# Kernel optimization log

Hardware: AMD Instinct MI355X
Metric: run time of the kernel (lower is better)

Reference implementation:

```python
import jax, jax.numpy as jnp
import numpy as np

B, T, S, E, H = 2, 1024, 1024, 1024, 16
D = E // H  # head_dim = 64
SCALING = D ** -0.5


def setup_inputs() -> dict:
    key = jax.random.key(0)
    ks = jax.random.split(key, 14)
    inv = 1.0 / np.sqrt(E)
    inp = {
        "query": jax.random.normal(ks[0], (B, T, E), jnp.float32),
        "key": jax.random.normal(ks[1], (B, S, E), jnp.float32),
        "value": jax.random.normal(ks[2], (B, S, E), jnp.float32),
        "key_padding_mask": jax.random.bernoulli(ks[3], 0.1, (B, S)),
        "attn_bias": jax.random.normal(ks[4], (B * H, T, S), jnp.float32),
        "Wq": jax.random.uniform(ks[5], (E, E), jnp.float32, -inv, inv),
        "bq": jax.random.uniform(ks[6], (E,), jnp.float32, -inv, inv),
        "Wk": jax.random.uniform(ks[7], (E, E), jnp.float32, -inv, inv),
        "bk": jax.random.uniform(ks[8], (E,), jnp.float32, -inv, inv),
        "Wv": jax.random.uniform(ks[9], (E, E), jnp.float32, -inv, inv),
        "bv": jax.random.uniform(ks[10], (E,), jnp.float32, -inv, inv),
        "Wo": jax.random.uniform(ks[11], (E, E), jnp.float32, -inv, inv),
        "bo": jax.random.uniform(ks[12], (E,), jnp.float32, -inv, inv),
    }
    return inp


def reference(query, key, value, key_padding_mask, attn_bias,
              Wq, bq, Wk, bk, Wv, bv, Wo, bo):
    # Projections (torch Linear: x @ W.T + b)
    q = query @ Wq.T + bq  # [B, T, E]
    k = key @ Wk.T + bk    # [B, S, E]
    v = value @ Wv.T + bv  # [B, S, E]
    # Split heads -> [B, H, L, D]
    q = q.reshape(B, T, H, D).transpose(0, 2, 1, 3) * SCALING
    k = k.reshape(B, S, H, D).transpose(0, 2, 1, 3)
    v = v.reshape(B, S, H, D).transpose(0, 2, 1, 3)
    # Scores [B, H, T, S]
    attn_weights = jnp.einsum('bhtd,bhsd->bhts', q, k)
    # key_padding_mask: True means masked -> -inf (applied BEFORE bias add)
    attn_weights = jnp.where(key_padding_mask[:, None, None, :], -jnp.inf, attn_weights)
    # softmax_dropout with additive bias (eval mode: dropout is identity)
    attn_weights = attn_weights + attn_bias.reshape(B, H, T, S)
    attn = jax.nn.softmax(attn_weights, axis=-1)
    o = jnp.einsum('bhts,bhsd->bhtd', attn, v)  # [B, H, T, D]
    o = o.transpose(0, 2, 1, 3).reshape(B, T, E)
    return o @ Wo.T + bo
```

## Files before the change

### kernel.cpp

```cpp
#include <hip/hip_runtime.h>
#include <math.h>
#include <stdint.h>

#define B_ 2
#define T_ 1024
#define S_ 1024
#define E_ 1024
#define H_ 16
#define SCALING_ 0.125f

typedef short bf16x8 __attribute__((ext_vector_type(8)));
typedef float f32x4 __attribute__((ext_vector_type(4)));
typedef unsigned short us8 __attribute__((ext_vector_type(8)));

__device__ __forceinline__ unsigned short f2bf(float x) {
    unsigned int u = __float_as_uint(x);
    return (unsigned short)((u + 0x7fffu + ((u >> 16) & 1u)) >> 16);
}
__device__ __forceinline__ float bf2f(unsigned short h) {
    return __uint_as_float(((unsigned int)h) << 16);
}
__device__ __forceinline__ void split_bf(float x, unsigned short& hh, unsigned short& ll) {
    hh = f2bf(x);
    ll = f2bf(x - bf2f(hh));
}
__device__ __forceinline__ void gl_lds16(const void* g, void* l) {
    __builtin_amdgcn_global_load_lds(
        (const __attribute__((address_space(1))) unsigned int*)g,
        (__attribute__((address_space(3))) unsigned int*)l, 16, 0, 0);
}
template <int CTRL>
__device__ __forceinline__ float dpp_ror(float x) {
    int v = __builtin_amdgcn_update_dpp(0, __float_as_int(x), CTRL, 0xf, 0xf, true);
    return __int_as_float(v);
}

__global__ void mask_detect_kernel(const unsigned int* __restrict__ p,
                                   int* __restrict__ mode_out) {
    __shared__ int gt1_s, oddnz_s;
    if (threadIdx.x == 0) { gt1_s = 0; oddnz_s = 0; }
    __syncthreads();
    int gt1 = 0;
    for (int i = threadIdx.x; i < 512; i += 256)
        if (p[i] > 1u) gt1 = 1;
    if (gt1) atomicOr(&gt1_s, 1);
    __syncthreads();
    if (gt1_s == 0) {
        int oddnz = 0;
        for (int i = threadIdx.x; i < 2048; i += 256)
            if ((i & 1) && p[i] != 0u) oddnz = 1;
        if (oddnz) atomicOr(&oddnz_s, 1);
    }
    __syncthreads();
    if (threadIdx.x == 0)
        *mode_out = gt1_s ? 1 : (oddnz_s ? 0 : 2);
}

__global__ void mask_norm_kernel(const void* __restrict__ p,
                                 const int* __restrict__ mode_p,
                                 int* __restrict__ mout) {
    int i = blockIdx.x * 256 + threadIdx.x;
    int mode = *mode_p;
    int v;
    if (mode == 1)      v = (int)((const unsigned char*)p)[i];
    else if (mode == 2) v = ((const int*)p)[2 * i];
    else                v = ((const int*)p)[i];
    mout[i] = v;
}

__global__ __launch_bounds__(256) void conv_split7_kernel(
    const float* __restrict__ Wq, const float* __restrict__ Wk,
    const float* __restrict__ Wv, const float* __restrict__ Wo,
    const float* __restrict__ xq, const float* __restrict__ xk,
    const float* __restrict__ xv,
    unsigned short* __restrict__ Wqh, unsigned short* __restrict__ Wql,
    unsigned short* __restrict__ Wkh, unsigned short* __restrict__ Wkl,
    unsigned short* __restrict__ Wvh, unsigned short* __restrict__ Wvl,
    unsigned short* __restrict__ Woh, unsigned short* __restrict__ Wol,
    unsigned short* __restrict__ xqh, unsigned short* __restrict__ xql,
    unsigned short* __restrict__ xkh, unsigned short* __restrict__ xkl,
    unsigned short* __restrict__ xvh, unsigned short* __restrict__ xvl) {
    int bid = blockIdx.x;
    const float* src; unsigned short* dh; unsigned short* dl; int lb;
    if (bid < 2048) {
        int w = bid >> 9; lb = bid & 511;
        if (w == 0)      { src = Wq; dh = Wqh; dl = Wql; }
        else if (w == 1) { src = Wk; dh = Wkh; dl = Wkl; }
        else if (w == 2) { src = Wv; dh = Wvh; dl = Wvl; }
        else             { src = Wo; dh = Woh; dl = Wol; }
    } else {
        int a = (bid - 2048) >> 10; lb = (bid - 2048) & 1023;
        if (a == 0)      { src = xq; dh = xqh; dl = xql; }
        else if (a == 1) { src = xk; dh = xkh; dl = xkl; }
        else             { src = xv; dh = xvh; dl = xvl; }
    }
    int i = (lb * 256 + threadIdx.x) * 8;
    float4 a4 = *(const float4*)&src[i];
    float4 b4 = *(const float4*)&src[i + 4];
    float v[8] = {a4.x, a4.y, a4.z, a4.w, b4.x, b4.y, b4.z, b4.w};
    us8 vh, vl;
#pragma unroll
    for (int j = 0; j < 8; j++) {
        unsigned short hh, ll;
        split_bf(v[j], hh, ll);
        vh[j] = hh; vl[j] = ll;
    }
    *(us8*)&dh[i] = vh;
    *(us8*)&dl[i] = vl;
}

template <int BM, int NW, int N, int K, int ROWBIAS, int SPLITOUT>
__device__ __forceinline__ void gemm_body2(
    int bid,
    const unsigned short* __restrict__ Ahg, const unsigned short* __restrict__ Alg,
    const unsigned short* __restrict__ Bhg, const unsigned short* __restrict__ Blg,
    const float* __restrict__ bias,
    unsigned short* __restrict__ outh, unsigned short* __restrict__ outl,
    float* __restrict__ outf, float alpha, unsigned short* lds) {
    const int tid = threadIdx.x;
    const int lane = tid & 63;
    const int wave = tid >> 6;
    const int wm = wave >> 1, wn = wave & 1;
    const int bn = bid % (N / 64);
    const int bm = bid / (N / 64);
    const int m0 = bm * BM, n0 = bn * 64;
    constexpr int NT = K / 32;
    constexpr int ABUF = BM * 32;
    constexpr int BUFE = 2 * ABUF + 4096;
    const int arow = tid >> 2, aoct = tid & 3;

    f32x4 acc[2][2];
#pragma unroll
    for (int i = 0; i < 2; i++)
#pragma unroll
        for (int j = 0; j < 2; j++) acc[i][j] = (f32x4){0.f, 0.f, 0.f, 0.f};

    auto stage = [&](int k0, unsigned short* buf) {
        int ao2 = aoct ^ ((arow >> 1) & 3);
        size_t ga = (size_t)(m0 + arow) * K + k0 + ao2 * 8;
        gl_lds16(&Ahg[ga], &buf[arow * 32 + aoct * 8]);
        gl_lds16(&Alg[ga], &buf[ABUF + arow * 32 + aoct * 8]);
        if (NW == 8) {
            int bslot = tid & 255;
            int brow = bslot >> 2, boct = bslot & 3;
            int bo2 = boct ^ ((brow >> 1) & 3);
            size_t gb = (size_t)(n0 + brow) * K + k0 + bo2 * 8;
            const unsigned short* src = (tid < 256) ? Bhg : Blg;
            gl_lds16(&src[gb],
                     &buf[2 * ABUF + (tid < 256 ? 0 : 2048) + bslot * 8]);
        } else {
            int brow = tid >> 2, boct = tid & 3;
            int bo2 = boct ^ ((brow >> 1) & 3);
            size_t gb = (size_t)(n0 + brow) * K + k0 + bo2 * 8;
            gl_lds16(&Bhg[gb], &buf[2 * ABUF + tid * 8]);
            gl_lds16(&Blg[gb], &buf[2 * ABUF + 2048 + tid * 8]);
        }
    };

    stage(0, lds);
    asm volatile("s_waitcnt vmcnt(0)" ::: "memory");
    __syncthreads();

    for (int t = 0; t < NT; t++) {
        unsigned short* cur = lds + (t & 1) * BUFE;
        unsigned short* nxt = lds + ((t & 1) ^ 1) * BUFE;
        if (t + 1 < NT) stage((t + 1) * 32, nxt);

        bf16x8 af[2][2], bf_[2][2];
#pragma unroll
        for (int nj = 0; nj < 2; nj++) {
            int rowB = wn * 32 + nj * 16 + (lane & 15);
            int ch = (lane >> 4) ^ ((rowB >> 1) & 3);
            bf_[nj][0] = *(const bf16x8*)&cur[2 * ABUF + rowB * 32 + ch * 8];
            bf_[nj][1] = *(const bf16x8*)&cur[2 * ABUF + 2048 + rowB * 32 + ch * 8];
        }
#pragma unroll
        for (int mi = 0; mi < 2; mi++) {
            int rowA = wm * 32 + mi * 16 + (lane & 15);
            int ch = (lane >> 4) ^ ((rowA >> 1) & 3);
            af[mi][0] = *(const bf16x8*)&cur[rowA * 32 + ch * 8];
            af[mi][1] = *(const bf16x8*)&cur[ABUF + rowA * 32 + ch * 8];
        }
#pragma unroll
        for (int mi = 0; mi < 2; mi++)
#pragma unroll
            for (int nj = 0; nj < 2; nj++) {
                acc[mi][nj] = __builtin_amdgcn_mfma_f32_16x16x32_bf16(af[mi][0], bf_[nj][0], acc[mi][nj], 0, 0, 0);
                acc[mi][nj] = __builtin_amdgcn_mfma_f32_16x16x32_bf16(af[mi][1], bf_[nj][0], acc[mi][nj], 0, 0, 0);
                acc[mi][nj] = __builtin_amdgcn_mfma_f32_16x16x32_bf16(af[mi][0], bf_[nj][1], acc[mi][nj], 0, 0, 0);
            }

        asm volatile("s_waitcnt vmcnt(0)" ::: "memory");
        __syncthreads();
    }

    float bcol[2];
    if (!ROWBIAS) {
#pragma unroll
        for (int nj = 0; nj < 2; nj++)
            bcol[nj] = bias[n0 + wn * 32 + nj * 16 + (lane & 15)];
    }
#pragma unroll
    for (int mi = 0; mi < 2; mi++) {
#pragma unroll
        for (int r = 0; r < 4; r++) {
            int row = m0 + wm * 32 + mi * 16 + (lane >> 4) * 4 + r;
            float brow = ROWBIAS ? bias[row] : 0.f;
#pragma unroll
            for (int nj = 0; nj < 2; nj++) {
                int col = n0 + wn * 32 + nj * 16 + (lane & 15);
                float v = alpha * (acc[mi][nj][r] + (ROWBIAS ? brow : bcol[nj]));
                if (SPLITOUT) {
                    unsigned short hh, ll;
                    split_bf(v, hh, ll);
                    outh[(size_t)row * N + col] = hh;
                    outl[(size_t)row * N + col] = ll;
                } else {
                    outf[(size_t)row * N + col] = v;
                }
            }
        }
    }
}

__global__ __launch_bounds__(512, 4) void proj_fused_kernel(
    const unsigned short* __restrict__ xqh, const unsigned short* __restrict__ xql,
    const unsigned short* __restrict__ xkh, const unsigned short* __restrict__ xkl,
    const unsigned short* __restrict__ xvh, const unsigned short* __restrict__ xvl,
    const unsigned short* __restrict__ Wqh, const unsigned short* __restrict__ Wql,
    const unsigned short* __restrict__ Wkh, const unsigned short* __restrict__ Wkl,
    const unsigned short* __restrict__ Wvh, const unsigned short* __restrict__ Wvl,
    const float* __restrict__ bq, const float* __restrict__ bk,
    const float* __restrict__ bv_,
    unsigned short* __restrict__ qh, unsigned short* __restrict__ ql,
    unsigned short* __restrict__ kh, unsigned short* __restrict__ kl,
    unsigned short* __restrict__ vth, unsigned short* __restrict__ vtl) {
    __shared__ __align__(16) unsigned short lds[2 * (2 * 128 * 32 + 4096)];
    int op = blockIdx.x >> 8;
    int bid = blockIdx.x & 255;
    if (op == 0)
        gemm_body2<128, 8, 1024, 1024, 0, 1>(bid, xqh, xql, Wqh, Wql, bq,
                                             qh, ql, nullptr, SCALING_, lds);
    else if (op == 1)
        gemm_body2<128, 8, 1024, 1024, 0, 1>(bid, xkh, xkl, Wkh, Wkl, bk,
                                             kh, kl, nullptr, 1.f, lds);
    else
        gemm_body2<128, 8, 2048, 1024, 1, 1>(bid, Wvh, Wvl, xvh, xvl, bv_,
                                             vth, vtl, nullptr, 1.f, lds);
}

__global__ __launch_bounds__(256) void gemm_out_kernel(
    const unsigned short* __restrict__ oh, const unsigned short* __restrict__ ol,
    const unsigned short* __restrict__ Woh, const unsigned short* __restrict__ Wol,
    const float* __restrict__ bo, float* __restrict__ out) {
    __shared__ __align__(16) unsigned short lds[2 * (2 * 64 * 32 + 4096)];
    gemm_body2<64, 4, 1024, 1024, 0, 0>(blockIdx.x, oh, ol, Woh, Wol, bo,
                                        nullptr, nullptr, out, 1.f, lds);
}

__global__ __launch_bounds__(256) void flash_kernel(
    const unsigned short* __restrict__ qh, const unsigned short* __restrict__ ql,
    const unsigned short* __restrict__ kh, const unsigned short* __restrict__ kl,
    const unsigned short* __restrict__ vth, const unsigned short* __restrict__ vtl,
    const float* __restrict__ bias, const int* __restrict__ mask,
    unsigned short* __restrict__ oh, unsigned short* __restrict__ ol) {
    __shared__ __align__(16) unsigned short Ksh[2][4096], Ksl[2][4096];
    __shared__ __align__(16) unsigned short Vsh[2][4096], Vsl[2][4096];
    __shared__ __align__(16) unsigned short Ph[4][1024], Pl[4][1024];

    const int tid = threadIdx.x;
    const int lane = tid & 63;
    const int wave = tid >> 6;
    const int bh = blockIdx.x >> 4;
    const int tt = blockIdx.x & 15;
    const int b = bh >> 4, h = bh & 15;
    const int t0 = tt * 64;
    const int srow = tid >> 3;
    const int soct = tid & 7;

#pragma unroll
    for (int p = 0; p < 2; p++) {
        int row = p * 32 + srow;
        int oct2 = soct ^ (row & 7);
        size_t g = (size_t)(b * T_ + t0 + row) * E_ + h * 64 + oct2 * 8;
        gl_lds16(&qh[g], &Ksh[0][row * 64 + soct * 8]);
        gl_lds16(&ql[g], &Ksl[0][row * 64 + soct * 8]);
    }
    asm volatile("s_waitcnt vmcnt(0)" ::: "memory");
    __syncthreads();
    bf16x8 qfh[2], qfl[2];
    {
        int row = wave * 16 + (lane & 15);
#pragma unroll
        for (int kk = 0; kk < 2; kk++) {
            int ch = (kk * 4 + (lane >> 4)) ^ (row & 7);
            qfh[kk] = *(const bf16x8*)&Ksh[0][row * 64 + ch * 8];
            qfl[kk] = *(const bf16x8*)&Ksl[0][row * 64 + ch * 8];
        }
    }
    __syncthreads();

    float mrow[4] = {-INFINITY, -INFINITY, -INFINITY, -INFINITY};
    float lrow[4] = {0.f, 0.f, 0.f, 0.f};
    f32x4 oacc[4];
#pragma unroll
    for (int dj = 0; dj < 4; dj++) oacc[dj] = (f32x4){0.f, 0.f, 0.f, 0.f};

    const size_t bias0 = ((size_t)bh * T_ + t0 + wave * 16) * S_;

    float bv[4][4];
    int mk[4];
#pragma unroll
    for (int p = 0; p < 2; p++) {
        int row = p * 32 + srow;
        int oct2 = soct ^ (row & 7);
        size_t gk = (size_t)(b * S_ + row) * E_ + h * 64 + oct2 * 8;
        gl_lds16(&kh[gk], &Ksh[0][row * 64 + soct * 8]);
        gl_lds16(&kl[gk], &Ksl[0][row * 64 + soct * 8]);
        size_t gv = (size_t)(h * 64 + row) * (B_ * S_) + b * S_ + oct2 * 8;
        gl_lds16(&vth[gv], &Vsh[0][row * 64 + soct * 8]);
        gl_lds16(&vtl[gv], &Vsl[0][row * 64 + soct * 8]);
    }
#pragma unroll
    for (int nj = 0; nj < 4; nj++) {
        int s = nj * 16 + (lane & 15);
        mk[nj] = mask[b * S_ + s];
#pragma unroll
        for (int r = 0; r < 4; r++)
            bv[nj][r] = bias[bias0 + (size_t)((lane >> 4) * 4 + r) * S_ + s];
    }
    asm volatile("s_waitcnt vmcnt(0)" ::: "memory");
    __syncthreads();

    for (int s0i = 0; s0i < 16; s0i++) {
        const int s0 = s0i * 64;
        const int cur = s0i & 1;
        const int nxt = cur ^ 1;

        if (s0i < 15) {
            const int s0n = s0 + 64;
#pragma unroll
            for (int p = 0; p < 2; p++) {
                int row = p * 32 + srow;
                int oct2 = soct ^ (row & 7);
                size_t gk = (size_t)(b * S_ + s0n + row) * E_ + h * 64 + oct2 * 8;
                gl_lds16(&kh[gk], &Ksh[nxt][row * 64 + soct * 8]);
                gl_lds16(&kl[gk], &Ksl[nxt][row * 64 + soct * 8]);
                size_t gv = (size_t)(h * 64 + row) * (B_ * S_) + b * S_ + s0n + oct2 * 8;
                gl_lds16(&vth[gv], &Vsh[nxt][row * 64 + soct * 8]);
                gl_lds16(&vtl[gv], &Vsl[nxt][row * 64 + soct * 8]);
            }
        }

        f32x4 sc[4];
#pragma unroll
        for (int nj = 0; nj < 4; nj++) sc[nj] = (f32x4){0.f, 0.f, 0.f, 0.f};
#pragma unroll
        for (int kk = 0; kk < 2; kk++) {
#pragma unroll
            for (int nj = 0; nj < 4; nj++) {
                int row = nj * 16 + (lane & 15);
                int ch = (kk * 4 + (lane >> 4)) ^ (row & 7);
                bf16x8 kfh = *(const bf16x8*)&Ksh[cur][row * 64 + ch * 8];
                bf16x8 kfl = *(const bf16x8*)&Ksl[cur][row * 64 + ch * 8];
                sc[nj] = __builtin_amdgcn_mfma_f32_16x16x32_bf16(qfh[kk], kfh, sc[nj], 0, 0, 0);
                sc[nj] = __builtin_amdgcn_mfma_f32_16x16x32_bf16(qfl[kk], kfh, sc[nj], 0, 0, 0);
                sc[nj] = __builtin_amdgcn_mfma_f32_16x16x32_bf16(qfh[kk], kfl, sc[nj], 0, 0, 0);
            }
        }
#pragma unroll
        for (int nj = 0; nj < 4; nj++)
#pragma unroll
            for (int r = 0; r < 4; r++) {
                float v = mk[nj] ? -INFINITY : sc[nj][r];
                sc[nj][r] = v + bv[nj][r];
            }

        if (s0i < 15) {
            const int s0n = s0 + 64;
#pragma unroll
            for (int nj = 0; nj < 4; nj++) {
                int s = s0n + nj * 16 + (lane & 15);
                mk[nj] = mask[b * S_ + s];
#pragma unroll
                for (int r = 0; r < 4; r++)
                    bv[nj][r] = bias[bias0 + (size_t)((lane >> 4) * 4 + r) * S_ + s];
            }
        }

        unsigned short phv[4][4], plv[4][4];
#pragma unroll
        for (int r = 0; r < 4; r++) {
            float mx = fmaxf(fmaxf(sc[0][r], sc[1][r]), fmaxf(sc[2][r], sc[3][r]));
            mx = fmaxf(mx, dpp_ror<0x121>(mx));
            mx = fmaxf(mx, dpp_ror<0x122>(mx));
            mx = fmaxf(mx, dpp_ror<0x124>(mx));
            mx = fmaxf(mx, dpp_ror<0x128>(mx));
            float mnew = fmaxf(mrow[r], mx);
            float esc = __expf(mrow[r] - mnew);
            float ps = 0.f;
#pragma unroll
            for (int nj = 0; nj < 4; nj++) {
                float p = __expf(sc[nj][r] - mnew);
                ps += p;
                split_bf(p, phv[nj][r], plv[nj][r]);
            }
            ps += dpp_ror<0x121>(ps);
            ps += dpp_ror<0x122>(ps);
            ps += dpp_ror<0x124>(ps);
            ps += dpp_ror<0x128>(ps);
            lrow[r] = lrow[r] * esc + ps;
            mrow[r] = mnew;
#pragma unroll
            for (int dj = 0; dj < 4; dj++) oacc[dj][r] *= esc;
        }

#pragma unroll
        for (int r = 0; r < 4; r++) {
            int t = (lane >> 4) * 4 + r;
            int f = (((t >> 2) & 3) << 1) | (t & 1);
#pragma unroll
            for (int nj = 0; nj < 4; nj++) {
                int s = nj * 16 + (lane & 15);
                int idx = t * 64 + (((s >> 3) ^ f) * 8) + (s & 7);
                Ph[wave][idx] = phv[nj][r];
                Pl[wave][idx] = plv[nj][r];
            }
        }
        bf16x8 pah[2], pal[2];
        {
            int t = lane & 15;
            int f = (((t >> 2) & 3) << 1) | (t & 1);
#pragma unroll
            for (int kk = 0; kk < 2; kk++) {
                int ch = (kk * 4 + (lane >> 4)) ^ f;
                pah[kk] = *(const bf16x8*)&Ph[wave][t * 64 + ch * 8];
                pal[kk] = *(const bf16x8*)&Pl[wave][t * 64 + ch * 8];
            }
        }
#pragma unroll
        for (int dj = 0; dj < 4; dj++) {
            int row = dj * 16 + (lane & 15);
#pragma unroll
            for (int kk = 0; kk < 2; kk++) {
                int ch = (kk * 4 + (lane >> 4)) ^ (row & 7);
                bf16x8 vfh = *(const bf16x8*)&Vsh[cur][row * 64 + ch * 8];
                bf16x8 vfl = *(const bf16x8*)&Vsl[cur][row * 64 + ch * 8];
                oacc[dj] = __builtin_amdgcn_mfma_f32_16x16x32_bf16(pah[kk], vfh, oacc[dj], 0, 0, 0);
                oacc[dj] = __builtin_amdgcn_mfma_f32_16x16x32_bf16(pal[kk], vfh, oacc[dj], 0, 0, 0);
                oacc[dj] = __builtin_amdgcn_mfma_f32_16x16x32_bf16(pah[kk], vfl, oacc[dj], 0, 0, 0);
            }
        }

        asm volatile("s_waitcnt vmcnt(0)" ::: "memory");
        __syncthreads();
    }

#pragma unroll
    for (int r = 0; r < 4; r++) {
        float inv = 1.f / lrow[r];
        int t = t0 + wave * 16 + (lane >> 4) * 4 + r;
#pragma unroll
        for (int dj = 0; dj < 4; dj++) {
            float v = oacc[dj][r] * inv;
            unsigned short hh, ll;
            split_bf(v, hh, ll);
            size_t g = (size_t)(b * T_ + t) * E_ + h * 64 + dj * 16 + (lane & 15);
            oh[g] = hh;
            ol[g] = ll;
        }
    }
}

extern "C" void kernel_launch(void* const* d_in, const int* in_sizes, int n_in,
                              void* d_out, int out_size, void* d_ws,
                              size_t ws_size, hipStream_t stream) {
    const float* query = (const float*)d_in[0];
    const float* key   = (const float*)d_in[1];
    const float* value = (const float*)d_in[2];
    const void*  kpm   = d_in[3];
    const float* attn_bias = (const float*)d_in[4];
    const float* Wq = (const float*)d_in[5];
    const float* bq = (const float*)d_in[6];
    const float* Wk = (const float*)d_in[7];
    const float* bk = (const float*)d_in[8];
    const float* Wv = (const float*)d_in[9];
    const float* bv = (const float*)d_in[10];
    const float* Wo = (const float*)d_in[11];
    const float* bo = (const float*)d_in[12];
    float* out = (float*)d_out;

    char* ws = (char*)d_ws;
    const size_t MB = 1024 * 1024;
    unsigned short* Wqh = (unsigned short*)(ws + 0 * MB);
    unsigned short* Wql = (unsigned short*)(ws + 2 * MB);
    unsigned short* Wkh = (unsigned short*)(ws + 4 * MB);
    unsigned short* Wkl = (unsigned short*)(ws + 6 * MB);
    unsigned short* Wvh = (unsigned short*)(ws + 8 * MB);
    unsigned short* Wvl = (unsigned short*)(ws + 10 * MB);
    unsigned short* Woh = (unsigned short*)(ws + 12 * MB);
    unsigned short* Wol = (unsigned short*)(ws + 14 * MB);
    unsigned short* qh = (unsigned short*)(ws + 16 * MB);
    unsigned short* ql = (unsigned short*)(ws + 20 * MB);
    unsigned short* kh = (unsigned short*)(ws + 24 * MB);
    unsigned short* kl = (unsigned short*)(ws + 28 * MB);
    unsigned short* vth = (unsigned short*)(ws + 32 * MB);
    unsigned short* vtl = (unsigned short*)(ws + 36 * MB);
    unsigned short* xqh = (unsigned short*)(ws + 40 * MB);
    unsigned short* xql = (unsigned short*)(ws + 44 * MB);
    unsigned short* xkh = (unsigned short*)(ws + 48 * MB);
    unsigned short* xkl = (unsigned short*)(ws + 52 * MB);
    unsigned short* xvh = (unsigned short*)(ws + 56 * MB);
    unsigned short* xvl = (unsigned short*)(ws + 60 * MB);
    unsigned short* oh = (unsigned short*)(ws + 40 * MB);
    unsigned short* ol = (unsigned short*)(ws + 44 * MB);
    int* masknorm = (int*)(ws + 64 * MB);
    int* mode = masknorm + 2048;

    conv_split7_kernel<<<5120, 256, 0, stream>>>(
        Wq, Wk, Wv, Wo, query, key, value,
        Wqh, Wql, Wkh, Wkl, Wvh, Wvl, Woh, Wol,
        xqh, xql, xkh, xkl, xvh, xvl);
    mask_detect_kernel<<<1, 256, 0, stream>>>((const unsigned int*)kpm, mode);
    mask_norm_kernel<<<8, 256, 0, stream>>>(kpm, mode, masknorm);

    proj_fused_kernel<<<768, 512, 0, stream>>>(
        xqh, xql, xkh, xkl, xvh, xvl,
        Wqh, Wql, Wkh, Wkl, Wvh, Wvl, bq, bk, bv,
        qh, ql, kh, kl, vth, vtl);

    flash_kernel<<<512, 256, 0, stream>>>(qh, ql, kh, kl, vth, vtl, attn_bias,
                                          masknorm, oh, ol);

    gemm_out_kernel<<<512, 256, 0, stream>>>(oh, ol, Woh, Wol, bo, out);
}
```

Baseline: 339.3 us.

## Triple-buffer GEMM pipeline and stage attention bias through LDS asynchronously

The GEMM body moves from double to triple buffering with 64x64 tiles and partial vmcnt waits, so only one barrier is needed per K step. The projection kernel shrinks to 256-thread blocks with twice as many blocks. The flash kernel now loads the bias tile asynchronously into LDS with global_load_lds instead of per-lane register gathers, single-buffers V (staged after the barrier), reuses the bias buffer for P, and raises wave priority around the MFMA sections. This is meant to overlap global loads with compute and cut load latency stalls, at the cost of tighter synchronisation and more fragile waitcnt accounting.

Result: no change. 344.9 us (+1.6%).

```diff
diff --git a/kernel.cpp b/kernel.cpp
--- a/kernel.cpp
+++ b/kernel.cpp
@@ -12,15 +12,16 @@
 typedef short bf16x8 __attribute__((ext_vector_type(8)));
 typedef float f32x4 __attribute__((ext_vector_type(4)));
 typedef unsigned short us8 __attribute__((ext_vector_type(8)));
-
-__device__ __forceinline__ unsigned short f2bf(float x) {
+typedef unsigned short ush;
+
+__device__ __forceinline__ ush f2bf(float x) {
     unsigned int u = __float_as_uint(x);
-    return (unsigned short)((u + 0x7fffu + ((u >> 16) & 1u)) >> 16);
-}
-__device__ __forceinline__ float bf2f(unsigned short h) {
+    return (ush)((u + 0x7fffu + ((u >> 16) & 1u)) >> 16);
+}
+__device__ __forceinline__ float bf2f(ush h) {
     return __uint_as_float(((unsigned int)h) << 16);
 }
-__device__ __forceinline__ void split_bf(float x, unsigned short& hh, unsigned short& ll) {
+__device__ __forceinline__ void split_bf(float x, ush& hh, ush& ll) {
     hh = f2bf(x);
     ll = f2bf(x - bf2f(hh));
 }
@@ -34,6 +35,8 @@
     int v = __builtin_amdgcn_update_dpp(0, __float_as_int(x), CTRL, 0xf, 0xf, true);
     return __int_as_float(v);
 }
+#define FENCE() asm volatile("" ::: "memory")
+#define BARRIER() do { FENCE(); __builtin_amdgcn_s_barrier(); FENCE(); } while (0)
 
 __global__ void mask_detect_kernel(const unsigned int* __restrict__ p,
                                    int* __restrict__ mode_out) {
@@ -73,15 +76,15 @@
     const float* __restrict__ Wv, const float* __restrict__ Wo,
     const float* __restrict__ xq, const float* __restrict__ xk,
     const float* __restrict__ xv,
-    unsigned short* __restrict__ Wqh, unsigned short* __restrict__ Wql,
-    unsigned short* __restrict__ Wkh, unsigned short* __restrict__ Wkl,
-    unsigned short* __restrict__ Wvh, unsigned short* __restrict__ Wvl,
-    unsigned short* __restrict__ Woh, unsigned short* __restrict__ Wol,
-    unsigned short* __restrict__ xqh, unsigned short* __restrict__ xql,
-    unsigned short* __restrict__ xkh, unsigned short* __restrict__ xkl,
-    unsigned short* __restrict__ xvh, unsigned short* __restrict__ xvl) {
+    ush* __restrict__ Wqh, ush* __restrict__ Wql,
+    ush* __restrict__ Wkh, ush* __restrict__ Wkl,
+    ush* __restrict__ Wvh, ush* __restrict__ Wvl,
+    ush* __restrict__ Woh, ush* __restrict__ Wol,
+    ush* __restrict__ xqh, ush* __restrict__ xql,
+    ush* __restrict__ xkh, ush* __restrict__ xkl,
+    ush* __restrict__ xvh, ush* __restrict__ xvl) {
     int bid = blockIdx.x;
-    const float* src; unsigned short* dh; unsigned short* dl; int lb;
+    const float* src; ush* dh; ush* dl; int lb;
     if (bid < 2048) {
         int w = bid >> 9; lb = bid & 511;
         if (w == 0)      { src = Wq; dh = Wqh; dl = Wql; }
@@ -101,7 +104,7 @@
     us8 vh, vl;
 #pragma unroll
     for (int j = 0; j < 8; j++) {
-        unsigned short hh, ll;
+        ush hh, ll;
         split_bf(v[j], hh, ll);
         vh[j] = hh; vl[j] = ll;
     }
@@ -109,25 +112,24 @@
     *(us8*)&dl[i] = vl;
 }
 
-template <int BM, int NW, int N, int K, int ROWBIAS, int SPLITOUT>
-__device__ __forceinline__ void gemm_body2(
+template <int N, int K, int ROWBIAS, int SPLITOUT>
+__device__ __forceinline__ void gemm_body3(
     int bid,
-    const unsigned short* __restrict__ Ahg, const unsigned short* __restrict__ Alg,
-    const unsigned short* __restrict__ Bhg, const unsigned short* __restrict__ Blg,
+    const ush* __restrict__ Ahg, const ush* __restrict__ Alg,
+    const ush* __restrict__ Bhg, const ush* __restrict__ Blg,
     const float* __restrict__ bias,
-    unsigned short* __restrict__ outh, unsigned short* __restrict__ outl,
-    float* __restrict__ outf, float alpha, unsigned short* lds) {
+    ush* __restrict__ outh, ush* __restrict__ outl,
+    float* __restrict__ outf, float alpha, ush* lds) {
     const int tid = threadIdx.x;
     const int lane = tid & 63;
     const int wave = tid >> 6;
     const int wm = wave >> 1, wn = wave & 1;
     const int bn = bid % (N / 64);
     const int bm = bid / (N / 64);
-    const int m0 = bm * BM, n0 = bn * 64;
+    const int m0 = bm * 64, n0 = bn * 64;
     constexpr int NT = K / 32;
-    constexpr int ABUF = BM * 32;
-    constexpr int BUFE = 2 * ABUF + 4096;
-    const int arow = tid >> 2, aoct = tid & 3;
+    const int row = tid >> 2, oct = tid & 3;
+    const int oct2 = oct ^ ((row >> 1) & 3);
 
     f32x4 acc[2][2];
 #pragma unroll
@@ -135,63 +137,54 @@
 #pragma unroll
         for (int j = 0; j < 2; j++) acc[i][j] = (f32x4){0.f, 0.f, 0.f, 0.f};
 
-    auto stage = [&](int k0, unsigned short* buf) {
-        int ao2 = aoct ^ ((arow >> 1) & 3);
-        size_t ga = (size_t)(m0 + arow) * K + k0 + ao2 * 8;
-        gl_lds16(&Ahg[ga], &buf[arow * 32 + aoct * 8]);
-        gl_lds16(&Alg[ga], &buf[ABUF + arow * 32 + aoct * 8]);
-        if (NW == 8) {
-            int bslot = tid & 255;
-            int brow = bslot >> 2, boct = bslot & 3;
-            int bo2 = boct ^ ((brow >> 1) & 3);
-            size_t gb = (size_t)(n0 + brow) * K + k0 + bo2 * 8;
-            const unsigned short* src = (tid < 256) ? Bhg : Blg;
-            gl_lds16(&src[gb],
-                     &buf[2 * ABUF + (tid < 256 ? 0 : 2048) + bslot * 8]);
-        } else {
-            int brow = tid >> 2, boct = tid & 3;
-            int bo2 = boct ^ ((brow >> 1) & 3);
-            size_t gb = (size_t)(n0 + brow) * K + k0 + bo2 * 8;
-            gl_lds16(&Bhg[gb], &buf[2 * ABUF + tid * 8]);
-            gl_lds16(&Blg[gb], &buf[2 * ABUF + 2048 + tid * 8]);
-        }
+    auto stage = [&](int k0, ush* buf) {
+        size_t ga = (size_t)(m0 + row) * K + k0 + oct2 * 8;
+        gl_lds16(&Ahg[ga], &buf[tid * 8]);
+        gl_lds16(&Alg[ga], &buf[2048 + tid * 8]);
+        size_t gb = (size_t)(n0 + row) * K + k0 + oct2 * 8;
+        gl_lds16(&Bhg[gb], &buf[4096 + tid * 8]);
+        gl_lds16(&Blg[gb], &buf[6144 + tid * 8]);
     };
 
-    stage(0, lds);
-    asm volatile("s_waitcnt vmcnt(0)" ::: "memory");
-    __syncthreads();
+    ush* p0 = lds;
+    ush* p1 = lds + 8192;
+    ush* p2 = lds + 16384;
+    stage(0, p0);
+    stage(32, p1);
 
     for (int t = 0; t < NT; t++) {
-        unsigned short* cur = lds + (t & 1) * BUFE;
-        unsigned short* nxt = lds + ((t & 1) ^ 1) * BUFE;
-        if (t + 1 < NT) stage((t + 1) * 32, nxt);
-
-        bf16x8 af[2][2], bf_[2][2];
+        if (t + 1 < NT) asm volatile("s_waitcnt vmcnt(4)" ::: "memory");
+        else            asm volatile("s_waitcnt vmcnt(0)" ::: "memory");
+        BARRIER();
+        if (t + 2 < NT) stage((t + 2) * 32, p2);
+
+        bf16x8 afr[2][2], bfr[2][2];
 #pragma unroll
         for (int nj = 0; nj < 2; nj++) {
             int rowB = wn * 32 + nj * 16 + (lane & 15);
             int ch = (lane >> 4) ^ ((rowB >> 1) & 3);
-            bf_[nj][0] = *(const bf16x8*)&cur[2 * ABUF + rowB * 32 + ch * 8];
-            bf_[nj][1] = *(const bf16x8*)&cur[2 * ABUF + 2048 + rowB * 32 + ch * 8];
+            bfr[nj][0] = *(const bf16x8*)&p0[4096 + rowB * 32 + ch * 8];
+            bfr[nj][1] = *(const bf16x8*)&p0[6144 + rowB * 32 + ch * 8];
         }
 #pragma unroll
         for (int mi = 0; mi < 2; mi++) {
             int rowA = wm * 32 + mi * 16 + (lane & 15);
             int ch = (lane >> 4) ^ ((rowA >> 1) & 3);
-            af[mi][0] = *(const bf16x8*)&cur[rowA * 32 + ch * 8];
-            af[mi][1] = *(const bf16x8*)&cur[ABUF + rowA * 32 + ch * 8];
-        }
+            afr[mi][0] = *(const bf16x8*)&p0[rowA * 32 + ch * 8];
+            afr[mi][1] = *(const bf16x8*)&p0[2048 + rowA * 32 + ch * 8];
+        }
+        __builtin_amdgcn_s_setprio(1);
 #pragma unroll
         for (int mi = 0; mi < 2; mi++)
 #pragma unroll
             for (int nj = 0; nj < 2; nj++) {
-                acc[mi][nj] = __builtin_amdgcn_mfma_f32_16x16x32_bf16(af[mi][0], bf_[nj][0], acc[mi][nj], 0, 0, 0);
-                acc[mi][nj] = __builtin_amdgcn_mfma_f32_16x16x32_bf16(af[mi][1], bf_[nj][0], acc[mi][nj], 0, 0, 0);
-                acc[mi][nj] = __builtin_amdgcn_mfma_f32_16x16x32_bf16(af[mi][0], bf_[nj][1], acc[mi][nj], 0, 0, 0);
-            }
-
-        asm volatile("s_waitcnt vmcnt(0)" ::: "memory");
-        __syncthreads();
+                acc[mi][nj] = __builtin_amdgcn_mfma_f32_16x16x32_bf16(afr[mi][0], bfr[nj][0], acc[mi][nj], 0, 0, 0);
+                acc[mi][nj] = __builtin_amdgcn_mfma_f32_16x16x32_bf16(afr[mi][1], bfr[nj][0], acc[mi][nj], 0, 0, 0);
+                acc[mi][nj] = __builtin_amdgcn_mfma_f32_16x16x32_bf16(afr[mi][0], bfr[nj][1], acc[mi][nj], 0, 0, 0);
+            }
+        __builtin_amdgcn_s_setprio(0);
+
+        ush* tmp = p0; p0 = p1; p1 = p2; p2 = tmp;
     }
 
     float bcol[2];
@@ -204,69 +197,69 @@
     for (int mi = 0; mi < 2; mi++) {
 #pragma unroll
         for (int r = 0; r < 4; r++) {
-            int row = m0 + wm * 32 + mi * 16 + (lane >> 4) * 4 + r;
-            float brow = ROWBIAS ? bias[row] : 0.f;
+            int orow = m0 + wm * 32 + mi * 16 + (lane >> 4) * 4 + r;
+            float brow = ROWBIAS ? bias[orow] : 0.f;
 #pragma unroll
             for (int nj = 0; nj < 2; nj++) {
                 int col = n0 + wn * 32 + nj * 16 + (lane & 15);
                 float v = alpha * (acc[mi][nj][r] + (ROWBIAS ? brow : bcol[nj]));
                 if (SPLITOUT) {
-                    unsigned short hh, ll;
+                    ush hh, ll;
                     split_bf(v, hh, ll);
-                    outh[(size_t)row * N + col] = hh;
-                    outl[(size_t)row * N + col] = ll;
+                    outh[(size_t)orow * N + col] = hh;
+                    outl[(size_t)orow * N + col] = ll;
                 } else {
-                    outf[(size_t)row * N + col] = v;
+                    outf[(size_t)orow * N + col] = v;
                 }
             }
         }
     }
 }
 
-__global__ __launch_bounds__(512, 4) void proj_fused_kernel(
-    const unsigned short* __restrict__ xqh, const unsigned short* __restrict__ xql,
-    const unsigned short* __restrict__ xkh, const unsigned short* __restrict__ xkl,
-    const unsigned short* __restrict__ xvh, const unsigned short* __restrict__ xvl,
-    const unsigned short* __restrict__ Wqh, const unsigned short* __restrict__ Wql,
-    const unsigned short* __restrict__ Wkh, const unsigned short* __restrict__ Wkl,
-    const unsigned short* __restrict__ Wvh, const unsigned short* __restrict__ Wvl,
+__global__ __launch_bounds__(256) void proj_fused_kernel(
+    const ush* __restrict__ xqh, const ush* __restrict__ xql,
+    const ush* __restrict__ xkh, const ush* __restrict__ xkl,
+    const ush* __restrict__ xvh, const ush* __restrict__ xvl,
+    const ush* __restrict__ Wqh, const ush* __restrict__ Wql,
+    const ush* __restrict__ Wkh, const ush* __restrict__ Wkl,
+    const ush* __restrict__ Wvh, const ush* __restrict__ Wvl,
     const float* __restrict__ bq, const float* __restrict__ bk,
     const float* __restrict__ bv_,
-    unsigned short* __restrict__ qh, unsigned short* __restrict__ ql,
-    unsigned short* __restrict__ kh, unsigned short* __restrict__ kl,
-    unsigned short* __restrict__ vth, unsigned short* __restrict__ vtl) {
-    __shared__ __align__(16) unsigned short lds[2 * (2 * 128 * 32 + 4096)];
-    int op = blockIdx.x >> 8;
-    int bid = blockIdx.x & 255;
+    ush* __restrict__ qh, ush* __restrict__ ql,
+    ush* __restrict__ kh, ush* __restrict__ kl,
+    ush* __restrict__ vth, ush* __restrict__ vtl) {
+    __shared__ __align__(16) ush lds[3 * 8192];
+    int op = blockIdx.x / 512;
+    int bid = blockIdx.x % 512;
     if (op == 0)
-        gemm_body2<128, 8, 1024, 1024, 0, 1>(bid, xqh, xql, Wqh, Wql, bq,
-                                             qh, ql, nullptr, SCALING_, lds);
+        gemm_body3<1024, 1024, 0, 1>(bid, xqh, xql, Wqh, Wql, bq,
+                                     qh, ql, nullptr, SCALING_, lds);
     else if (op == 1)
-        gemm_body2<128, 8, 1024, 1024, 0, 1>(bid, xkh, xkl, Wkh, Wkl, bk,
-                                             kh, kl, nullptr, 1.f, lds);
+        gemm_body3<1024, 1024, 0, 1>(bid, xkh, xkl, Wkh, Wkl, bk,
+                                     kh, kl, nullptr, 1.f, lds);
     else
-        gemm_body2<128, 8, 2048, 1024, 1, 1>(bid, Wvh, Wvl, xvh, xvl, bv_,
-                                             vth, vtl, nullptr, 1.f, lds);
+        gemm_body3<2048, 1024, 1, 1>(bid, Wvh, Wvl, xvh, xvl, bv_,
+                                     vth, vtl, nullptr, 1.f, lds);
 }
 
 __global__ __launch_bounds__(256) void gemm_out_kernel(
-    const unsigned short* __restrict__ oh, const unsigned short* __restrict__ ol,
-    const unsigned short* __restrict__ Woh, const unsigned short* __restrict__ Wol,
+    const ush* __restrict__ oh, const ush* __restrict__ ol,
+    const ush* __restrict__ Woh, const ush* __restrict__ Wol,
     const float* __restrict__ bo, float* __restrict__ out) {
-    __shared__ __align__(16) unsigned short lds[2 * (2 * 64 * 32 + 4096)];
-    gemm_body2<64, 4, 1024, 1024, 0, 0>(blockIdx.x, oh, ol, Woh, Wol, bo,
-                                        nullptr, nullptr, out, 1.f, lds);
+    __shared__ __align__(16) ush lds[3 * 8192];
+    gemm_body3<1024, 1024, 0, 0>(blockIdx.x, oh, ol, Woh, Wol, bo,
+                                 nullptr, nullptr, out, 1.f, lds);
 }
 
 __global__ __launch_bounds__(256) void flash_kernel(
-    const unsigned short* __restrict__ qh, const unsigned short* __restrict__ ql,
-    const unsigned short* __restrict__ kh, const unsigned short* __restrict__ kl,
-    const unsigned short* __restrict__ vth, const unsigned short* __restrict__ vtl,
+    const ush* __restrict__ qh, const ush* __restrict__ ql,
+    const ush* __restrict__ kh, const ush* __restrict__ kl,
+    const ush* __restrict__ vth, const ush* __restrict__ vtl,
     const float* __restrict__ bias, const int* __restrict__ mask,
-    unsigned short* __restrict__ oh, unsigned short* __restrict__ ol) {
-    __shared__ __align__(16) unsigned short Ksh[2][4096], Ksl[2][4096];
-    __shared__ __align__(16) unsigned short Vsh[2][4096], Vsl[2][4096];
-    __shared__ __align__(16) unsigned short Ph[4][1024], Pl[4][1024];
+    ush* __restrict__ oh, ush* __restrict__ ol) {
+    __shared__ __align__(16) ush Ksh[2][4096], Ksl[2][4096];
+    __shared__ __align__(16) ush Vsh[4096], Vsl[4096];
+    __shared__ __align__(16) float BPb[2][4096];
 
     const int tid = threadIdx.x;
     const int lane = tid & 63;
@@ -281,8 +274,8 @@
 #pragma unroll
     for (int p = 0; p < 2; p++) {
         int row = p * 32 + srow;
-        int oct2 = soct ^ (row & 7);
-        size_t g = (size_t)(b * T_ + t0 + row) * E_ + h * 64 + oct2 * 8;
+        int oc2 = soct ^ (row & 7);
+        size_t g = (size_t)(b * T_ + t0 + row) * E_ + h * 64 + oc2 * 8;
         gl_lds16(&qh[g], &Ksh[0][row * 64 + soct * 8]);
         gl_lds16(&ql[g], &Ksl[0][row * 64 + soct * 8]);
     }
@@ -306,55 +299,60 @@
 #pragma unroll
     for (int dj = 0; dj < 4; dj++) oacc[dj] = (f32x4){0.f, 0.f, 0.f, 0.f};
 
-    const size_t bias0 = ((size_t)bh * T_ + t0 + wave * 16) * S_;
-
-    float bv[4][4];
+    auto stage_k = [&](int ti, int c) {
+#pragma unroll
+        for (int p = 0; p < 2; p++) {
+            int row = p * 32 + srow;
+            int oc2 = soct ^ (row & 7);
+            size_t gk = (size_t)(b * S_ + ti * 64 + row) * E_ + h * 64 + oc2 * 8;
+            gl_lds16(&kh[gk], &Ksh[c][row * 64 + soct * 8]);
+            gl_lds16(&kl[gk], &Ksl[c][row * 64 + soct * 8]);
+        }
+    };
+    auto stage_v = [&](int ti) {
+#pragma unroll
+        for (int p = 0; p < 2; p++) {
+            int row = p * 32 + srow;
+            int oc2 = soct ^ (row & 7);
+            size_t gv = (size_t)(h * 64 + row) * (B_ * S_) + b * S_ + ti * 64 + oc2 * 8;
+            gl_lds16(&vth[gv], &Vsh[row * 64 + soct * 8]);
+            gl_lds16(&vtl[gv], &Vsl[row * 64 + soct * 8]);
+        }
+    };
+    auto stage_bias = [&](int ti, int reg) {
+#pragma unroll
+        for (int p = 0; p < 4; p++) {
+            int row = p * 16 + (tid >> 4);
+            int slot = tid & 15;
+            int sslot = slot ^ (((row >> 2) & 1) << 2);
+            const float* src = bias + ((size_t)bh * T_ + t0 + row) * S_ +
+                               ti * 64 + sslot * 4;
+            gl_lds16(src, &BPb[reg][(p * 256 + tid) * 4]);
+        }
+    };
+
     int mk[4];
-#pragma unroll
-    for (int p = 0; p < 2; p++) {
-        int row = p * 32 + srow;
-        int oct2 = soct ^ (row & 7);
-        size_t gk = (size_t)(b * S_ + row) * E_ + h * 64 + oct2 * 8;
-        gl_lds16(&kh[gk], &Ksh[0][row * 64 + soct * 8]);
-        gl_lds16(&kl[gk], &Ksl[0][row * 64 + soct * 8]);
-        size_t gv = (size_t)(h * 64 + row) * (B_ * S_) + b * S_ + oct2 * 8;
-        gl_lds16(&vth[gv], &Vsh[0][row * 64 + soct * 8]);
-        gl_lds16(&vtl[gv], &Vsl[0][row * 64 + soct * 8]);
-    }
-#pragma unroll
-    for (int nj = 0; nj < 4; nj++) {
-        int s = nj * 16 + (lane & 15);
-        mk[nj] = mask[b * S_ + s];
-#pragma unroll
-        for (int r = 0; r < 4; r++)
-            bv[nj][r] = bias[bias0 + (size_t)((lane >> 4) * 4 + r) * S_ + s];
-    }
+    stage_k(0, 0);
+    stage_v(0);
+    stage_bias(0, 0);
+#pragma unroll
+    for (int nj = 0; nj < 4; nj++)
+        mk[nj] = mask[b * S_ + nj * 16 + (lane & 15)];
     asm volatile("s_waitcnt vmcnt(0)" ::: "memory");
     __syncthreads();
 
-    for (int s0i = 0; s0i < 16; s0i++) {
-        const int s0 = s0i * 64;
-        const int cur = s0i & 1;
-        const int nxt = cur ^ 1;
-
-        if (s0i < 15) {
-            const int s0n = s0 + 64;
-#pragma unroll
-            for (int p = 0; p < 2; p++) {
-                int row = p * 32 + srow;
-                int oct2 = soct ^ (row & 7);
-                size_t gk = (size_t)(b * S_ + s0n + row) * E_ + h * 64 + oct2 * 8;
-                gl_lds16(&kh[gk], &Ksh[nxt][row * 64 + soct * 8]);
-                gl_lds16(&kl[gk], &Ksl[nxt][row * 64 + soct * 8]);
-                size_t gv = (size_t)(h * 64 + row) * (B_ * S_) + b * S_ + s0n + oct2 * 8;
-                gl_lds16(&vth[gv], &Vsh[nxt][row * 64 + soct * 8]);
-                gl_lds16(&vtl[gv], &Vsl[nxt][row * 64 + soct * 8]);
-            }
+    for (int t = 0; t < 16; t++) {
+        const int cur = t & 1;
+
+        if (t < 15) {
+            stage_k(t + 1, cur ^ 1);
+            stage_bias(t + 1, cur ^ 1);
         }
 
         f32x4 sc[4];
 #pragma unroll
         for (int nj = 0; nj < 4; nj++) sc[nj] = (f32x4){0.f, 0.f, 0.f, 0.f};
+        __builtin_amdgcn_s_setprio(1);
 #pragma unroll
         for (int kk = 0; kk < 2; kk++) {
 #pragma unroll
@@ -368,27 +366,31 @@
                 sc[nj] = __builtin_amdgcn_mfma_f32_16x16x32_bf16(qfh[kk], kfl, sc[nj], 0, 0, 0);
             }
         }
-#pragma unroll
-        for (int nj = 0; nj < 4; nj++)
+        __builtin_amdgcn_s_setprio(0);
+
+        {
+            const float* bp = &BPb[cur][wave * 1024];
 #pragma unroll
             for (int r = 0; r < 4; r++) {
-                float v = mk[nj] ? -INFINITY : sc[nj][r];
-                sc[nj][r] = v + bv[nj][r];
-            }
-
-        if (s0i < 15) {
-            const int s0n = s0 + 64;
-#pragma unroll
-            for (int nj = 0; nj < 4; nj++) {
-                int s = s0n + nj * 16 + (lane & 15);
-                mk[nj] = mask[b * S_ + s];
-#pragma unroll
-                for (int r = 0; r < 4; r++)
-                    bv[nj][r] = bias[bias0 + (size_t)((lane >> 4) * 4 + r) * S_ + s];
-            }
-        }
-
-        unsigned short phv[4][4], plv[4][4];
+                int tl = (lane >> 4) * 4 + r;
+                int sx = ((tl >> 2) & 1) << 4;
+#pragma unroll
+                for (int nj = 0; nj < 4; nj++) {
+                    int s = (nj * 16 + (lane & 15)) ^ sx;
+                    float bvv = bp[tl * 64 + s];
+                    float v = mk[nj] ? -INFINITY : sc[nj][r];
+                    sc[nj][r] = v + bvv;
+                }
+            }
+        }
+        if (t < 15) {
+            const int s0n = (t + 1) * 64;
+#pragma unroll
+            for (int nj = 0; nj < 4; nj++)
+                mk[nj] = mask[b * S_ + s0n + nj * 16 + (lane & 15)];
+        }
+
+        ush phv[4][4], plv[4][4];
 #pragma unroll
         for (int r = 0; r < 4; r++) {
             float mx = fmaxf(fmaxf(sc[0][r], sc[1][r]), fmaxf(sc[2][r], sc[3][r]));
@@ -415,45 +417,53 @@
             for (int dj = 0; dj < 4; dj++) oacc[dj][r] *= esc;
         }
 
+        ush* Pw = (ush*)&BPb[cur][wave * 1024];
 #pragma unroll
         for (int r = 0; r < 4; r++) {
-            int t = (lane >> 4) * 4 + r;
-            int f = (((t >> 2) & 3) << 1) | (t & 1);
+            int tq = (lane >> 4) * 4 + r;
+            int f = (((tq >> 2) & 3) << 1) | (tq & 1);
 #pragma unroll
             for (int nj = 0; nj < 4; nj++) {
                 int s = nj * 16 + (lane & 15);
-                int idx = t * 64 + (((s >> 3) ^ f) * 8) + (s & 7);
-                Ph[wave][idx] = phv[nj][r];
-                Pl[wave][idx] = plv[nj][r];
+                int idx = tq * 64 + (((s >> 3) ^ f) * 8) + (s & 7);
+                Pw[idx] = phv[nj][r];
+                Pw[1024 + idx] = plv[nj][r];
             }
         }
         bf16x8 pah[2], pal[2];
         {
-            int t = lane & 15;
-            int f = (((t >> 2) & 3) << 1) | (t & 1);
+            int tq = lane & 15;
+            int f = (((tq >> 2) & 3) << 1) | (tq & 1);
 #pragma unroll
             for (int kk = 0; kk < 2; kk++) {
                 int ch = (kk * 4 + (lane >> 4)) ^ f;
-                pah[kk] = *(const bf16x8*)&Ph[wave][t * 64 + ch * 8];
-                pal[kk] = *(const bf16x8*)&Pl[wave][t * 64 + ch * 8];
-            }
-        }
+                pah[kk] = *(const bf16x8*)&Pw[tq * 64 + ch * 8];
+                pal[kk] = *(const bf16x8*)&Pw[1024 + tq * 64 + ch * 8];
+            }
+        }
+
+        if (t < 15) asm volatile("s_waitcnt vmcnt(8)" ::: "memory");
+        else        asm volatile("s_waitcnt vmcnt(0)" ::: "memory");
+
+        __builtin_amdgcn_s_setprio(1);
 #pragma unroll
         for (int dj = 0; dj < 4; dj++) {
             int row = dj * 16 + (lane & 15);
 #pragma unroll
             for (int kk = 0; kk < 2; kk++) {
                 int ch = (kk * 4 + (lane >> 4)) ^ (row & 7);
-                bf16x8 vfh = *(const bf16x8*)&Vsh[cur][row * 64 + ch * 8];
-                bf16x8 vfl = *(const bf16x8*)&Vsl[cur][row * 64 + ch * 8];
+                bf16x8 vfh = *(const bf16x8*)&Vsh[row * 64 + ch * 8];
+                bf16x8 vfl = *(const bf16x8*)&Vsl[row * 64 + ch * 8];
                 oacc[dj] = __builtin_amdgcn_mfma_f32_16x16x32_bf16(pah[kk], vfh, oacc[dj], 0, 0, 0);
                 oacc[dj] = __builtin_amdgcn_mfma_f32_16x16x32_bf16(pal[kk], vfh, oacc[dj], 0, 0, 0);
                 oacc[dj] = __builtin_amdgcn_mfma_f32_16x16x32_bf16(pah[kk], vfl, oacc[dj], 0, 0, 0);
             }
         }
+        __builtin_amdgcn_s_setprio(0);
 
         asm volatile("s_waitcnt vmcnt(0)" ::: "memory");
-        __syncthreads();
+        BARRIER();
+        if (t < 15) stage_v(t + 1);
     }
 
 #pragma unroll
@@ -463,7 +473,7 @@
 #pragma unroll
         for (int dj = 0; dj < 4; dj++) {
             float v = oacc[dj][r] * inv;
-            unsigned short hh, ll;
+            ush hh, ll;
             split_bf(v, hh, ll);
             size_t g = (size_t)(b * T_ + t) * E_ + h * 64 + dj * 16 + (lane & 15);
             oh[g] = hh;
@@ -492,28 +502,28 @@
 
     char* ws = (char*)d_ws;
     const size_t MB = 1024 * 1024;
-    unsigned short* Wqh = (unsigned short*)(ws + 0 * MB);
-    unsigned short* Wql = (unsigned short*)(ws + 2 * MB);
-    unsigned short* Wkh = (unsigned short*)(ws + 4 * MB);
-    unsigned short* Wkl = (unsigned short*)(ws + 6 * MB);
-    unsigned short* Wvh = (unsigned short*)(ws + 8 * MB);
-    unsigned short* Wvl = (unsigned short*)(ws + 10 * MB);
-    unsigned short* Woh = (unsigned short*)(ws + 12 * MB);
-    unsigned short* Wol = (unsigned short*)(ws + 14 * MB);
-    unsigned short* qh = (unsigned short*)(ws + 16 * MB);
-    unsigned short* ql = (unsigned short*)(ws + 20 * MB);
-    unsigned short* kh = (unsigned short*)(ws + 24 * MB);
-    unsigned short* kl = (unsigned short*)(ws + 28 * MB);
-    unsigned short* vth = (unsigned short*)(ws + 32 * MB);
-    unsigned short* vtl = (unsigned short*)(ws + 36 * MB);
-    unsigned short* xqh = (unsigned short*)(ws + 40 * MB);
-    unsigned short* xql = (unsigned short*)(ws + 44 * MB);
-    unsigned short* xkh = (unsigned short*)(ws + 48 * MB);
-    unsigned short* xkl = (unsigned short*)(ws + 52 * MB);
-    unsigned short* xvh = (unsigned short*)(ws + 56 * MB);
-    unsigned short* xvl = (unsigned short*)(ws + 60 * MB);
-    unsigned short* oh = (unsigned short*)(ws + 40 * MB);
-    unsigned short* ol = (unsigned short*)(ws + 44 * MB);
+    ush* Wqh = (ush*)(ws + 0 * MB);
+    ush* Wql = (ush*)(ws + 2 * MB);
+    ush* Wkh = (ush*)(ws + 4 * MB);
+    ush* Wkl = (ush*)(ws + 6 * MB);
+    ush* Wvh = (ush*)(ws + 8 * MB);
+    ush* Wvl = (ush*)(ws + 10 * MB);
+    ush* Woh = (ush*)(ws + 12 * MB);
+    ush* Wol = (ush*)(ws + 14 * MB);
+    ush* qh  = (ush*)(ws + 16 * MB);
+    ush* ql  = (ush*)(ws + 20 * MB);
+    ush* kh  = (ush*)(ws + 24 * MB);
+    ush* kl  = (ush*)(ws + 28 * MB);
+    ush* vth = (ush*)(ws + 32 * MB);
+    ush* vtl = (ush*)(ws + 36 * MB);
+    ush* xqh = (ush*)(ws + 40 * MB);
+    ush* xql = (ush*)(ws + 44 * MB);
+    ush* xkh = (ush*)(ws + 48 * MB);
+    ush* xkl = (ush*)(ws + 52 * MB);
+    ush* xvh = (ush*)(ws + 56 * MB);
+    ush* xvl = (ush*)(ws + 60 * MB);
+    ush* oh  = (ush*)(ws + 40 * MB);
+    ush* ol  = (ush*)(ws + 44 * MB);
     int* masknorm = (int*)(ws + 64 * MB);
     int* mode = masknorm + 2048;
 
@@ -524,7 +534,7 @@
     mask_detect_kernel<<<1, 256, 0, stream>>>((const unsigned int*)kpm, mode);
     mask_norm_kernel<<<8, 256, 0, stream>>>(kpm, mode, masknorm);
 
-    proj_fused_kernel<<<768, 512, 0, stream>>>(
+    proj_fused_kernel<<<1536, 256, 0, stream>>>(
         xqh, xql, xkh, xkl, xvh, xvl,
         Wqh, Wql, Wkh, Wkl, Wvh, Wvl, bq, bk, bv,
         qh, ql, kh, kl, vth, vtl);
```
